# Performance work log

Measured on AMD Instinct MI355X. Metric: run time of the kernel, lower is better.

## Reference

```python
import jax, jax.numpy as jnp
import numpy as np

K_DIM = 1024
N_HEADS = 16
HEAD = K_DIM // N_HEADS


def setup_inputs() -> dict:
    key = jax.random.key(0)
    kx, kq, kk, kv, ko = jax.random.split(key, 5)
    b, t = 2, 2048
    scale = 1.0 / np.sqrt(K_DIM)
    x = jax.random.normal(kx, (b, t, K_DIM), dtype=jnp.float32)
    # nn.Linear(k, k, bias=False): y = x @ W.T, W has shape [k, k]
    Wq = jax.random.normal(kq, (K_DIM, K_DIM), dtype=jnp.float32) * scale
    Wk = jax.random.normal(kk, (K_DIM, K_DIM), dtype=jnp.float32) * scale
    Wv = jax.random.normal(kv, (K_DIM, K_DIM), dtype=jnp.float32) * scale
    Wo = jax.random.normal(ko, (K_DIM, K_DIM), dtype=jnp.float32) * scale
    return {"x": x, "Wq": Wq, "Wk": Wk, "Wv": Wv, "Wo": Wo}


def reference(x, Wq, Wk, Wv, Wo):
    b, t, k = x.shape
    h, hs = N_HEADS, HEAD
    # projections (torch Linear: x @ W.T), split heads -> [b, h, t, hs]
    Q = (x @ Wq.T).reshape(b, t, h, hs).transpose(0, 2, 1, 3)
    Kt = (x @ Wk.T).reshape(b, t, h, hs).transpose(0, 2, 1, 3)
    V = (x @ Wv.T).reshape(b, t, h, hs).transpose(0, 2, 1, 3)
    # NOTE: original scales by sqrt(k) (model dim), not sqrt(head_size)
    scores = jnp.einsum('bhqd,bhkd->bhqk', Q, Kt) / jnp.sqrt(jnp.asarray(k, x.dtype))
    W = jax.nn.softmax(scores, axis=-1)
    O = jnp.einsum('bhqk,bhkd->bhqd', W, V)  # [b, h, t, hs]
    O = O.transpose(0, 2, 1, 3).reshape(b, t, k)
    return O @ Wo.T
```

## Files before the change

### kernel.cpp

```cpp
#include <hip/hip_runtime.h>
#include <hip/hip_bf16.h>

#define N_HEADS 16
#define HEAD 64
#define B_SZ 2
#define T_SZ 2048
#define KD 1024
#define M_TOT (B_SZ * T_SZ)

typedef short bf16x8 __attribute__((ext_vector_type(8)));
typedef short bf16x4 __attribute__((ext_vector_type(4)));
typedef float f32x4  __attribute__((ext_vector_type(4)));

#define MFMA32(a, b, c) __builtin_amdgcn_mfma_f32_16x16x32_bf16((a), (b), (c), 0, 0, 0)

#if __has_builtin(__builtin_amdgcn_mfma_f32_16x16x16bf16_1k)
__device__ __forceinline__ f32x4 MFMA16(bf16x4 a, bf16x4 b, f32x4 c) {
    return __builtin_amdgcn_mfma_f32_16x16x16bf16_1k(a, b, c, 0, 0, 0);
}
#elif __has_builtin(__builtin_amdgcn_mfma_f32_16x16x16_bf16)
__device__ __forceinline__ f32x4 MFMA16(bf16x4 a, bf16x4 b, f32x4 c) {
    return __builtin_amdgcn_mfma_f32_16x16x16_bf16(a, b, c, 0, 0, 0);
}
#else
__device__ __forceinline__ f32x4 MFMA16(bf16x4 a, bf16x4 b, f32x4 c) {
    asm volatile("v_mfma_f32_16x16x16_bf16 %0, %1, %2, %0"
                 : "+v"(c) : "v"(a), "v"(b));
    return c;
}
#endif

__device__ __forceinline__ ushort f2bf(float f) {
    __hip_bfloat16 h = __float2bfloat16(f);
    return *reinterpret_cast<ushort*>(&h);
}

__device__ __forceinline__ float exp2fast(float x) {
#if __has_builtin(__builtin_amdgcn_exp2f)
    return __builtin_amdgcn_exp2f(x);
#else
    return exp2f(x);
#endif
}

__device__ __forceinline__ void gl2lds16(const ushort* g, void* l) {
    __builtin_amdgcn_global_load_lds(
        (const __attribute__((address_space(1))) unsigned int*)g,
        (__attribute__((address_space(3))) unsigned int*)l, 16, 0, 0);
}

__global__ void cvt_all(const float* __restrict__ x,
                        const float* __restrict__ Wq, const float* __restrict__ Wk,
                        const float* __restrict__ Wv, const float* __restrict__ Wo,
                        ushort* __restrict__ xb, ushort* __restrict__ wb) {
    const int NX = (M_TOT * KD) / 4;
    const int NW = (KD * KD) / 4;
    int i = blockIdx.x * blockDim.x + threadIdx.x;
    float4 v;
    ushort* dst;
    if (i < NX) {
        v = reinterpret_cast<const float4*>(x)[i];
        dst = xb + (size_t)i * 4;
    } else {
        int j = i - NX;
        int w = j >> 18;
        int r = j & (NW - 1);
        const float* s = (w == 0) ? Wq : (w == 1) ? Wk : (w == 2) ? Wv : Wo;
        v = reinterpret_cast<const float4*>(s)[r];
        dst = wb + (size_t)w * KD * KD + (size_t)r * 4;
    }
    ushort4 o;
    o.x = f2bf(v.x); o.y = f2bf(v.y); o.z = f2bf(v.z); o.w = f2bf(v.w);
    *reinterpret_cast<ushort4*>(dst) = o;
}

template<int MODE>
__global__ __launch_bounds__(256) void gemm_bt(const ushort* __restrict__ A,
                                               const ushort* __restrict__ Bm,
                                               void* __restrict__ Cv) {
    const int bm = blockIdx.x;
    const int bn = blockIdx.y;
    __shared__ alignas(128) char As[16384];
    __shared__ alignas(128) char Bs[16384];
    const int tid = threadIdx.x;
    const int lane = tid & 63;
    const int w = tid >> 6;
    const int wr = w >> 1, wc = w & 1;
    const int r15 = lane & 15, q4 = lane >> 4;

    const int sl8 = lane >> 3;
    const int scol = (((lane & 7) * 16) ^ (sl8 << 4)) >> 1;

    f32x4 acc[4][4] = {};

    for (int k0 = 0; k0 < 1024; k0 += 64) {
        #pragma unroll
        for (int rr = 0; rr < 4; ++rr) {
            int r = rr * 32 + w * 8 + sl8;
            gl2lds16(A  + (size_t)(bm * 128 + r) * 1024 + k0 + scol, &As[(rr * 32 + w * 8) * 128]);
            gl2lds16(Bm + (size_t)(bn * 128 + r) * 1024 + k0 + scol, &Bs[(rr * 32 + w * 8) * 128]);
        }
        asm volatile("s_waitcnt vmcnt(0)" ::: "memory");
        __syncthreads();

        #pragma unroll
        for (int kk = 0; kk < 2; ++kk) {
            bf16x8 af[4], bfr[4];
            #pragma unroll
            for (int m = 0; m < 4; ++m) {
                int row = wr * 64 + m * 16 + r15;
                af[m] = *(const bf16x8*)(&As[row * 128 + ((kk * 64 + q4 * 16) ^ ((row & 7) << 4))]);
            }
            #pragma unroll
            for (int n = 0; n < 4; ++n) {
                int row = wc * 64 + n * 16 + r15;
                bfr[n] = *(const bf16x8*)(&Bs[row * 128 + ((kk * 64 + q4 * 16) ^ ((row & 7) << 4))]);
            }
            #pragma unroll
            for (int m = 0; m < 4; ++m)
                #pragma unroll
                for (int n = 0; n < 4; ++n)
                    acc[m][n] = MFMA32(af[m], bfr[n], acc[m][n]);
        }
        __syncthreads();
    }

    const int row0 = bm * 128 + wr * 64;
    const int col0 = bn * 128 + wc * 64;
    if (MODE == 0) {
        ushort* Qbase = (ushort*)Cv;
        const size_t seg = (size_t)32 * 2048 * 64;
        #pragma unroll
        for (int m = 0; m < 4; ++m)
            #pragma unroll
            for (int n = 0; n < 4; ++n) {
                int col = col0 + n * 16 + r15;
                int which = col >> 10;
                int rem = col & 1023;
                int head = rem >> 6;
                int d = rem & 63;
                int row_base = row0 + m * 16 + q4 * 4;
                int bidx = row_base >> 11;
                int t = row_base & 2047;
                int bh_ = bidx * 16 + head;
                if (which == 2) {
                    ushort4 o;
                    o.x = f2bf(acc[m][n][0]); o.y = f2bf(acc[m][n][1]);
                    o.z = f2bf(acc[m][n][2]); o.w = f2bf(acc[m][n][3]);
                    *(ushort4*)(&Qbase[2 * seg + ((size_t)bh_ * 64 + d) * 2048 + t]) = o;
                } else {
                    float sc = (which == 0) ? 0.045084439f : 1.0f;
                    #pragma unroll
                    for (int i = 0; i < 4; ++i)
                        Qbase[(size_t)which * seg + ((size_t)bh_ * 2048 + t + i) * 64 + d] =
                            f2bf(acc[m][n][i] * sc);
                }
            }
    } else {
        float* C = (float*)Cv;
        #pragma unroll
        for (int m = 0; m < 4; ++m)
            #pragma unroll
            for (int n = 0; n < 4; ++n)
                #pragma unroll
                for (int i = 0; i < 4; ++i) {
                    int row = row0 + m * 16 + q4 * 4 + i;
                    int col = col0 + n * 16 + r15;
                    C[(size_t)row * 1024 + col] = acc[m][n][i];
                }
    }
}

__global__ __launch_bounds__(1024) void attn_fwd(const ushort* __restrict__ Qh,
                                                 const ushort* __restrict__ Kh,
                                                 const ushort* __restrict__ Vt,
                                                 ushort* __restrict__ Ob) {
    const int bh = blockIdx.x;
    const int qt = blockIdx.y;
    const int tid = threadIdx.x;
    const int lane = tid & 63, w = tid >> 6;
    const int grp = w >> 3, wl = w & 7;
    const int r15 = lane & 15, q4 = lane >> 4;

    const ushort* Qp = Qh + (size_t)bh * T_SZ * HEAD;
    const ushort* Kp = Kh + (size_t)bh * T_SZ * HEAD;
    const ushort* Vp = Vt + (size_t)bh * HEAD * T_SZ;

    __shared__ alignas(16) char SMEM[65536];
    char* Kbuf = SMEM + grp * 32768;
    char* Vbuf = Kbuf + 16384;

    const int srow = wl * 8 + (lane >> 3);
    const int sslot = (lane & 7) * 16;
    const int ssb = (sslot ^ ((srow & 7) << 4)) >> 1;
    const int kvbase = grp << 10;

    const int q0 = qt * 256 + wl * 32;
    bf16x8 qf[2][2];
    #pragma unroll
    for (int cc = 0; cc < 2; ++cc) {
        qf[cc][0] = *(const bf16x8*)(&Qp[(size_t)(q0 + cc * 16 + r15) * 64 + q4 * 8]);
        qf[cc][1] = *(const bf16x8*)(&Qp[(size_t)(q0 + cc * 16 + r15) * 64 + 32 + q4 * 8]);
    }

    float l_[2] = {0.f, 0.f};
    f32x4 acc[2][4] = {};

    #define STAGE(buf, kv0)                                                      \
        {                                                                        \
            gl2lds16(Kp + (size_t)(kvbase + (kv0) + srow) * 64 + ssb,            \
                     Kbuf + (buf) * 8192 + wl * 8 * 128);                        \
            gl2lds16(Vp + (size_t)srow * 2048 + kvbase + (kv0) + ssb,            \
                     Vbuf + (buf) * 8192 + wl * 8 * 128);                        \
        }

    STAGE(0, 0);
    asm volatile("s_waitcnt vmcnt(0)" ::: "memory");
    __syncthreads();

    int cur = 0;
    for (int it = 0; it < 16; ++it) {
        if (it < 15) STAGE(cur ^ 1, (it + 1) * 64);

        const char* Ks = Kbuf + cur * 8192;
        const char* Vs = Vbuf + cur * 8192;

        bf16x8 kf[4][2];
        #pragma unroll
        for (int t4 = 0; t4 < 4; ++t4) {
            int row = t4 * 16 + r15;
            int sw = (row & 7) << 4;
            kf[t4][0] = *(const bf16x8*)(&Ks[row * 128 + ((q4 * 16) ^ sw)]);
            kf[t4][1] = *(const bf16x8*)(&Ks[row * 128 + ((64 + q4 * 16) ^ sw)]);
        }
        bf16x4 vf[4][4];
        #pragma unroll
        for (int dt = 0; dt < 4; ++dt) {
            int row = dt * 16 + r15;
            int sw = (row & 7) << 4;
            #pragma unroll
            for (int t4 = 0; t4 < 4; ++t4)
                vf[t4][dt] = *(const bf16x4*)(&Vs[row * 128 + ((t4 * 32 + q4 * 8) ^ sw)]);
        }

        f32x4 z[2][4];
        #pragma unroll
        for (int cc = 0; cc < 2; ++cc)
            #pragma unroll
            for (int t4 = 0; t4 < 4; ++t4) {
                f32x4 zz = {};
                zz = MFMA32(kf[t4][0], qf[cc][0], zz);
                zz = MFMA32(kf[t4][1], qf[cc][1], zz);
                z[cc][t4] = zz;
            }

        bf16x4 pb[2][4];
        #pragma unroll
        for (int cc = 0; cc < 2; ++cc) {
            float rst[4];
            #pragma unroll
            for (int t4 = 0; t4 < 4; ++t4) {
                float p0 = exp2fast(z[cc][t4][0]);
                float p1 = exp2fast(z[cc][t4][1]);
                float p2 = exp2fast(z[cc][t4][2]);
                float p3 = exp2fast(z[cc][t4][3]);
                pb[cc][t4][0] = (short)f2bf(p0);
                pb[cc][t4][1] = (short)f2bf(p1);
                pb[cc][t4][2] = (short)f2bf(p2);
                pb[cc][t4][3] = (short)f2bf(p3);
                rst[t4] = (p0 + p1) + (p2 + p3);
            }
            l_[cc] += (rst[0] + rst[1]) + (rst[2] + rst[3]);
        }

        #pragma unroll
        for (int t4 = 0; t4 < 4; ++t4)
            #pragma unroll
            for (int dt = 0; dt < 4; ++dt)
                #pragma unroll
                for (int cc = 0; cc < 2; ++cc)
                    acc[cc][dt] = MFMA16(vf[t4][dt], pb[cc][t4], acc[cc][dt]);

        asm volatile("s_waitcnt vmcnt(0)" ::: "memory");
        __syncthreads();
        cur ^= 1;
    }
    #undef STAGE

    {
        float* MB = (float*)SMEM;
        #pragma unroll
        for (int rnd = 0; rnd < 2; ++rnd) {
            __syncthreads();
            if (grp == 1 && (wl >> 2) == rnd) {
                float* p = MB + (((wl & 3) * 64 + lane) * 34);
                #pragma unroll
                for (int cc = 0; cc < 2; ++cc)
                    #pragma unroll
                    for (int dt = 0; dt < 4; ++dt) {
                        *(float2*)(p + (cc * 4 + dt) * 4)     = make_float2(acc[cc][dt][0], acc[cc][dt][1]);
                        *(float2*)(p + (cc * 4 + dt) * 4 + 2) = make_float2(acc[cc][dt][2], acc[cc][dt][3]);
                    }
                *(float2*)(p + 32) = make_float2(l_[0], l_[1]);
            }
            __syncthreads();
            if (grp == 0 && (wl >> 2) == rnd) {
                const float* p = MB + (((wl & 3) * 64 + lane) * 34);
                #pragma unroll
                for (int cc = 0; cc < 2; ++cc)
                    #pragma unroll
                    for (int dt = 0; dt < 4; ++dt)
                        #pragma unroll
                        for (int i = 0; i < 4; ++i)
                            acc[cc][dt][i] += p[(cc * 4 + dt) * 4 + i];
                l_[0] += p[32];
                l_[1] += p[33];
            }
        }
    }

    if (grp == 0) {
        const int b = bh >> 4, h = bh & 15;
        #pragma unroll
        for (int cc = 0; cc < 2; ++cc) {
            float lf = l_[cc];
            lf += __shfl_xor(lf, 16, 64);
            lf += __shfl_xor(lf, 32, 64);
            float inv = 1.0f / lf;
            int q = q0 + cc * 16 + r15;
            #pragma unroll
            for (int dt = 0; dt < 4; ++dt) {
                ushort4 o;
                o.x = f2bf(acc[cc][dt][0] * inv);
                o.y = f2bf(acc[cc][dt][1] * inv);
                o.z = f2bf(acc[cc][dt][2] * inv);
                o.w = f2bf(acc[cc][dt][3] * inv);
                *(ushort4*)(&Ob[((size_t)(b * T_SZ + q)) * KD + h * HEAD + dt * 16 + q4 * 4]) = o;
            }
        }
    }
}

extern "C" void kernel_launch(void* const* d_in, const int* in_sizes, int n_in,
                              void* d_out, int out_size, void* d_ws, size_t ws_size,
                              hipStream_t stream) {
    const float* x  = (const float*)d_in[0];
    const float* Wq = (const float*)d_in[1];
    const float* Wk = (const float*)d_in[2];
    const float* Wv = (const float*)d_in[3];
    const float* Wo = (const float*)d_in[4];

    char* ws = (char*)d_ws;
    const size_t MB = 1024 * 1024;
    ushort* xb    = (ushort*)(ws + 0);
    ushort* Wqkvb = (ushort*)(ws + 8  * MB);
    ushort* Wob   = Wqkvb + 3 * (size_t)KD * KD;
    ushort* Qh    = (ushort*)(ws + 16 * MB);
    ushort* Kh    = (ushort*)(ws + 24 * MB);
    ushort* VhT   = (ushort*)(ws + 32 * MB);
    ushort* Ob    = (ushort*)(ws + 40 * MB);

    {
        int total4 = (M_TOT * KD) / 4 + KD * KD;
        cvt_all<<<total4 / 256, 256, 0, stream>>>(x, Wq, Wk, Wv, Wo, xb, Wqkvb);
    }

    gemm_bt<0><<<dim3(32, 24), 256, 0, stream>>>(xb, Wqkvb, (void*)Qh);

    attn_fwd<<<dim3(32, 8), 1024, 0, stream>>>(Qh, Kh, VhT, Ob);

    gemm_bt<1><<<dim3(32, 8), 256, 0, stream>>>(Ob, Wob, d_out);
}
```

Measured before the change: 117.7 us.

## Stage Q/K epilogue through LDS for coalesced stores; split O-proj GEMM into smaller tiles

```diff
diff --git a/kernel.cpp b/kernel.cpp
--- a/kernel.cpp
+++ b/kernel.cpp
@@ -74,10 +74,9 @@
     *reinterpret_cast<ushort4*>(dst) = o;
 }
 
-template<int MODE>
-__global__ __launch_bounds__(256) void gemm_bt(const ushort* __restrict__ A,
-                                               const ushort* __restrict__ Bm,
-                                               void* __restrict__ Cv) {
+__global__ __launch_bounds__(256) void gemm_qkv(const ushort* __restrict__ A,
+                                                const ushort* __restrict__ Bm,
+                                                ushort* __restrict__ Qbase) {
     const int bm = blockIdx.x;
     const int bn = blockIdx.y;
     __shared__ alignas(128) char As[16384];
@@ -125,17 +124,17 @@
         __syncthreads();
     }
 
+    const size_t seg = (size_t)32 * 2048 * 64;
+    const int which = bn >> 3;
     const int row0 = bm * 128 + wr * 64;
-    const int col0 = bn * 128 + wc * 64;
-    if (MODE == 0) {
-        ushort* Qbase = (ushort*)Cv;
-        const size_t seg = (size_t)32 * 2048 * 64;
+    const int col0w = bn * 128 + wc * 64;
+
+    if (which == 2) {
         #pragma unroll
         for (int m = 0; m < 4; ++m)
             #pragma unroll
             for (int n = 0; n < 4; ++n) {
-                int col = col0 + n * 16 + r15;
-                int which = col >> 10;
+                int col = col0w + n * 16 + r15;
                 int rem = col & 1023;
                 int head = rem >> 6;
                 int d = rem & 63;
@@ -143,32 +142,103 @@
                 int bidx = row_base >> 11;
                 int t = row_base & 2047;
                 int bh_ = bidx * 16 + head;
-                if (which == 2) {
-                    ushort4 o;
-                    o.x = f2bf(acc[m][n][0]); o.y = f2bf(acc[m][n][1]);
-                    o.z = f2bf(acc[m][n][2]); o.w = f2bf(acc[m][n][3]);
-                    *(ushort4*)(&Qbase[2 * seg + ((size_t)bh_ * 64 + d) * 2048 + t]) = o;
-                } else {
-                    float sc = (which == 0) ? 0.045084439f : 1.0f;
-                    #pragma unroll
-                    for (int i = 0; i < 4; ++i)
-                        Qbase[(size_t)which * seg + ((size_t)bh_ * 2048 + t + i) * 64 + d] =
-                            f2bf(acc[m][n][i] * sc);
+                ushort4 o;
+                o.x = f2bf(acc[m][n][0]); o.y = f2bf(acc[m][n][1]);
+                o.z = f2bf(acc[m][n][2]); o.w = f2bf(acc[m][n][3]);
+                *(ushort4*)(&Qbase[2 * seg + ((size_t)bh_ * 64 + d) * 2048 + t]) = o;
+            }
+    } else {
+        const float sc = (which == 0) ? 0.045084439f : 1.0f;
+        char* ep = ((w & 2) ? (char*)Bs : (char*)As) + (w & 1) * 8192;
+        #pragma unroll
+        for (int m = 0; m < 4; ++m)
+            #pragma unroll
+            for (int n = 0; n < 4; ++n)
+                #pragma unroll
+                for (int i = 0; i < 4; ++i) {
+                    int row = m * 16 + q4 * 4 + i;
+                    int dby = (n * 16 + r15) * 2;
+                    *(ushort*)(ep + row * 128 + (dby ^ ((row & 7) << 4))) =
+                        f2bf(acc[m][n][i] * sc);
                 }
-            }
-    } else {
-        float* C = (float*)Cv;
-        #pragma unroll
-        for (int m = 0; m < 4; ++m)
-            #pragma unroll
-            for (int n = 0; n < 4; ++n)
-                #pragma unroll
-                for (int i = 0; i < 4; ++i) {
-                    int row = row0 + m * 16 + q4 * 4 + i;
-                    int col = col0 + n * 16 + r15;
-                    C[(size_t)row * 1024 + col] = acc[m][n][i];
-                }
-    }
+        const int head = (col0w & 1023) >> 6;
+        #pragma unroll
+        for (int j = 0; j < 8; ++j) {
+            int row = (lane >> 3) + j * 8;
+            bf16x8 vv = *(const bf16x8*)(ep + row * 128 +
+                                         (((lane & 7) * 16) ^ ((row & 7) << 4)));
+            int grow = row0 + row;
+            int bidx = grow >> 11;
+            int t = grow & 2047;
+            *(bf16x8*)(&Qbase[(size_t)which * seg +
+                              (((size_t)(bidx * 16 + head) * 2048 + t) * 64) + (lane & 7) * 8]) = vv;
+        }
+    }
+}
+
+__global__ __launch_bounds__(256) void gemm_o(const ushort* __restrict__ A,
+                                              const ushort* __restrict__ Bm,
+                                              float* __restrict__ C) {
+    const int bm = blockIdx.x;
+    const int bn = blockIdx.y;
+    __shared__ alignas(128) char As[16384];
+    __shared__ alignas(128) char Bs[8192];
+    const int tid = threadIdx.x;
+    const int lane = tid & 63;
+    const int w = tid >> 6;
+    const int wr = w >> 1, wc = w & 1;
+    const int r15 = lane & 15, q4 = lane >> 4;
+    const int sl8 = lane >> 3;
+    const int scol = (((lane & 7) * 16) ^ (sl8 << 4)) >> 1;
+
+    f32x4 acc[4][2] = {};
+
+    for (int k0 = 0; k0 < 1024; k0 += 64) {
+        #pragma unroll
+        for (int rr = 0; rr < 4; ++rr) {
+            int r = w * 32 + rr * 8 + sl8;
+            gl2lds16(A + (size_t)(bm * 128 + r) * 1024 + k0 + scol, &As[(w * 32 + rr * 8) * 128]);
+        }
+        #pragma unroll
+        for (int rr = 0; rr < 2; ++rr) {
+            int r = w * 16 + rr * 8 + sl8;
+            gl2lds16(Bm + (size_t)(bn * 64 + r) * 1024 + k0 + scol, &Bs[(w * 16 + rr * 8) * 128]);
+        }
+        asm volatile("s_waitcnt vmcnt(0)" ::: "memory");
+        __syncthreads();
+
+        #pragma unroll
+        for (int kk = 0; kk < 2; ++kk) {
+            bf16x8 af[4], bfr[2];
+            #pragma unroll
+            for (int m = 0; m < 4; ++m) {
+                int row = wr * 64 + m * 16 + r15;
+                af[m] = *(const bf16x8*)(&As[row * 128 + ((kk * 64 + q4 * 16) ^ ((row & 7) << 4))]);
+            }
+            #pragma unroll
+            for (int n = 0; n < 2; ++n) {
+                int row = wc * 32 + n * 16 + r15;
+                bfr[n] = *(const bf16x8*)(&Bs[row * 128 + ((kk * 64 + q4 * 16) ^ ((row & 7) << 4))]);
+            }
+            #pragma unroll
+            for (int m = 0; m < 4; ++m)
+                #pragma unroll
+                for (int n = 0; n < 2; ++n)
+                    acc[m][n] = MFMA32(af[m], bfr[n], acc[m][n]);
+        }
+        __syncthreads();
+    }
+
+    const int row0 = bm * 128 + wr * 64;
+    const int col0 = bn * 64 + wc * 32;
+    #pragma unroll
+    for (int m = 0; m < 4; ++m)
+        #pragma unroll
+        for (int n = 0; n < 2; ++n)
+            #pragma unroll
+            for (int i = 0; i < 4; ++i)
+                C[(size_t)(row0 + m * 16 + q4 * 4 + i) * 1024 + col0 + n * 16 + r15] =
+                    acc[m][n][i];
 }
 
 __global__ __launch_bounds__(1024) void attn_fwd(const ushort* __restrict__ Qh,
@@ -365,9 +435,9 @@
         cvt_all<<<total4 / 256, 256, 0, stream>>>(x, Wq, Wk, Wv, Wo, xb, Wqkvb);
     }
 
-    gemm_bt<0><<<dim3(32, 24), 256, 0, stream>>>(xb, Wqkvb, (void*)Qh);
+    gemm_qkv<<<dim3(32, 24), 256, 0, stream>>>(xb, Wqkvb, Qh);
 
     attn_fwd<<<dim3(32, 8), 1024, 0, stream>>>(Qh, Kh, VhT, Ob);
 
-    gemm_bt<1><<<dim3(32, 8), 256, 0, stream>>>(Ob, Wob, d_out);
-}
+    gemm_o<<<dim3(32, 16), 256, 0, stream>>>(Ob, Wob, (float*)d_out);
+}
```

Result: faster. 112.3 us (-4.6%).
